# Optimization experiments

Hardware: AMD Instinct MI355X
Metric: run time of the kernel (lower is better)

Reference implementation:

```python
import jax, jax.numpy as jnp
import numpy as np
import math

B, N, D = 8, 2048, 64


def setup_inputs() -> dict:
    key = jax.random.key(0)
    kq, kk, kv, kd = jax.random.split(key, 4)
    Q = jax.random.normal(kq, (B, N, D), dtype=jnp.float32)
    K = jax.random.normal(kk, (B, N, D), dtype=jnp.float32)
    V = jax.random.normal(kv, (B, N, D), dtype=jnp.float32)
    dist_matrix = jax.random.uniform(kd, (N, N), dtype=jnp.float32)
    return {"Q": Q, "K": K, "V": V, "dist_matrix": dist_matrix}


def rescale_distance_matrix(dist_matrix):
    # (1 + e^1) / (1 + exp(1 - dist))
    c = 1.0
    return (c + math.e) / (c + jnp.exp(c - dist_matrix))


def reference(Q, K, V, dist_matrix):
    d_k = K.shape[-1]
    inv_sqrt_dk = 1.0 / math.sqrt(d_k)
    # [B, N, N] raw attention logits
    qk = jnp.einsum("bnd,bmd->bnm", Q, K)
    # ReLU then multiply by rescaled distance matrix [N, N] on the right
    scores = jnp.matmul(jax.nn.relu(qk), rescale_distance_matrix(dist_matrix)) * inv_sqrt_dk
    attn = jax.nn.softmax(scores, axis=-1)
    context = jnp.einsum("bnm,bmd->bnd", attn, V)
    return context
```

## Files before the change

kernel.cpp:

```cpp
#include <hip/hip_runtime.h>


typedef _Float16 f16;
typedef _Float16 f16x8 __attribute__((ext_vector_type(8)));
typedef float    f32x4 __attribute__((ext_vector_type(4)));

#define AS1C(p) ((const __attribute__((address_space(1))) void*)(p))
#define AS3(p)  ((__attribute__((address_space(3))) void*)(p))

__device__ __forceinline__ f16x8 cvt_f16x8(float4 a, float4 b){
  f16x8 v;
  v[0]=(f16)a.x; v[1]=(f16)a.y; v[2]=(f16)a.z; v[3]=(f16)a.w;
  v[4]=(f16)b.x; v[5]=(f16)b.y; v[6]=(f16)b.z; v[7]=(f16)b.w;
  return v;
}

__launch_bounds__(256, 2)
__global__ void k_qk(const float* __restrict__ Q, const float* __restrict__ Km,
                     const float* __restrict__ V, const float* __restrict__ Dm,
                     f16* __restrict__ Ph, f16* __restrict__ RhT,
                     f16* __restrict__ VhT){
  __shared__ char shm[36864];
  const int bid = blockIdx.x;
  const int t = threadIdx.x;

  if (bid >= 2048){
    f16* tl = (f16*)shm;
    const int c = t & 63, g = t >> 6;
    if (bid < 3072){
      const int pid = bid - 2048;
      const int k0 = (pid & 31)*64, m0 = (pid >> 5)*64;
#pragma unroll
      for (int i=0;i<16;++i){
        int k = g*16 + i;
        float d = Dm[(size_t)(k0 + k)*2048 + m0 + c];
        tl[k*65 + c] = (f16)(3.7182818284590452f / (1.0f + __expf(1.0f - d)));
      }
      __syncthreads();
#pragma unroll
      for (int i=0;i<16;++i){
        int m = g*16 + i;
        RhT[(size_t)(m0 + m)*2048 + k0 + c] = tl[c*65 + m];
      }
    } else {
      const int pid = bid - 3072;
      const int m0 = (pid & 31)*64, b = pid >> 5;
#pragma unroll
      for (int i=0;i<16;++i){
        int m = g*16 + i;
        tl[m*65 + c] = (f16)V[((size_t)b*2048 + m0 + m)*64 + c];
      }
      __syncthreads();
#pragma unroll
      for (int i=0;i<16;++i){
        int d = g*16 + i;
        VhT[((size_t)b*64 + d)*2048 + m0 + c] = tl[c*65 + d];
      }
    }
    return;
  }

  f16* Qt = (f16*)shm;
  f16* Kt = (f16*)(shm + 18432);
  f16* Tt = (f16*)shm;

  const int w = t>>6, l = t&63, lr = l&15, q = l>>4;
  const int m0 = (bid & 15)*128, n0 = ((bid>>4) & 15)*128, b = bid >> 8;
  const int wr = (w>>1)*64, wc = (w&1)*64;
  const float* Qb = Q  + ((size_t)b*2048 + n0)*64;
  const float* Kb = Km + ((size_t)b*2048 + m0)*64;

  const int sr = t>>3, sc = t&7;
#pragma unroll
  for (int j=0;j<4;++j){
    int row = sr + 32*j;
    const float* p  = Qb + (size_t)row*64 + sc*8;
    *(f16x8*)(Qt + row*72 + sc*8) = cvt_f16x8(*(const float4*)p, *(const float4*)(p+4));
    const float* pk = Kb + (size_t)row*64 + sc*8;
    *(f16x8*)(Kt + row*72 + sc*8) = cvt_f16x8(*(const float4*)pk, *(const float4*)(pk+4));
  }
  __syncthreads();

  f32x4 acc[4][4] = {};
#pragma unroll
  for (int kc=0;kc<2;++kc){
    f16x8 af[4], bf[4];
#pragma unroll
    for (int ti=0;ti<4;++ti) af[ti] = *(const f16x8*)(Qt + (wr+16*ti+lr)*72 + kc*32 + q*8);
#pragma unroll
    for (int tj=0;tj<4;++tj) bf[tj] = *(const f16x8*)(Kt + (wc+16*tj+lr)*72 + kc*32 + q*8);
#pragma unroll
    for (int ti=0;ti<4;++ti)
#pragma unroll
      for (int tj=0;tj<4;++tj)
        acc[ti][tj] = __builtin_amdgcn_mfma_f32_16x16x32_f16(af[ti], bf[tj], acc[ti][tj], 0,0,0);
  }
  __syncthreads();
#pragma unroll
  for (int ti=0;ti<4;++ti)
#pragma unroll
    for (int tj=0;tj<4;++tj)
#pragma unroll
      for (int r=0;r<4;++r)
        Tt[(wr+16*ti+4*q+r)*136 + wc+16*tj+lr] = (f16)(fmaxf(acc[ti][tj][r],0.f)*0.125f);
  __syncthreads();
  const int g16 = t&15, r0 = t>>4;
#pragma unroll
  for (int j=0;j<8;++j){
    int row = r0 + 16*j;
    *(f16x8*)(Ph + ((size_t)b*2048 + n0 + row)*2048 + m0 + g16*8) =
        *(const f16x8*)(Tt + row*136 + g16*8);
  }
}

__launch_bounds__(256, 2)
__global__ void k_attn(const f16* __restrict__ Ph, const f16* __restrict__ RhT,
                       const f16* __restrict__ VhT, f16* __restrict__ Op,
                       float* __restrict__ mp, float* __restrict__ lp){
  __shared__ char smem[49152];
  f16*  Pbuf = (f16*)smem;
  f16*  Rbuf = (f16*)(smem + 16384);
  f16*  El   = (f16*)smem;
  float* stat_max = (float*)(smem + 33792);
  float* stat_sum = (float*)(smem + 34816);

  const int t = threadIdx.x, w = t>>6, l = t&63, lr = l&15, q = l>>4;
  const int bid = blockIdx.x;
  const int jq = bid & 7, nbb = bid >> 3, b = nbb & 7, nb = nbb >> 3;
  const int n0 = nb*128, jg = jq*256;
  const int wc = w*64;

  const f16* Pblk = Ph  + ((size_t)b*2048 + n0)*2048;
  const f16* Vb   = VhT + (size_t)b*64*2048;

  const f16* srcP[2];
  const f16* srcR[4];
#pragma unroll
  for (int i=0;i<2;++i){
    int slot = i*256 + t, row = slot>>2, g = slot&3;
    srcP[i] = Pblk + (size_t)row*2048 + (g ^ ((row>>1)&3))*8;
  }
#pragma unroll
  for (int i=0;i<4;++i){
    int slot = i*256 + t, row = slot>>2, g = slot&3;
    srcR[i] = RhT + (size_t)(jg + row)*2048 + (g ^ ((row>>1)&3))*8;
  }

  auto stage = [&](int kc){
    const int cb = kc & 1, k0 = kc*32;
#pragma unroll
    for (int i=0;i<2;++i)
      __builtin_amdgcn_global_load_lds(AS1C(srcP[i] + k0),
                                       AS3(Pbuf + cb*4096 + i*2048 + w*512), 16, 0, 0);
#pragma unroll
    for (int i=0;i<4;++i)
      __builtin_amdgcn_global_load_lds(AS1C(srcR[i] + k0),
                                       AS3(Rbuf + cb*8192 + i*2048 + w*512), 16, 0, 0);
  };

  const int swz = (lr>>1)&3;
  f32x4 acc[8][4] = {};
  f32x4 Oacc[2][2][2] = {};

  stage(0);
#pragma unroll 2
  for (int kc = 0; kc < 64; ++kc){
    __syncthreads();
    if (kc < 63) stage(kc+1);
    const int cb = kc & 1;
    const f16* Pb = Pbuf + cb*4096;
    const f16* Rb = Rbuf + cb*8192;
    f16x8 bf[4];
#pragma unroll
    for (int tj=0;tj<4;++tj)
      bf[tj] = *(const f16x8*)(Rb + (wc + 16*tj + lr)*32 + (q ^ swz)*8);
#pragma unroll
    for (int ti=0;ti<8;++ti){
      f16x8 af = *(const f16x8*)(Pb + (16*ti + lr)*32 + (q ^ swz)*8);
#pragma unroll
      for (int tj=0;tj<4;++tj)
        acc[ti][tj] = __builtin_amdgcn_mfma_f32_16x16x32_f16(af, bf[tj], acc[ti][tj], 0,0,0);
    }
  }
  __syncthreads();

#pragma unroll
  for (int p=0;p<2;++p){
    float pm[4][4];
#pragma unroll
    for (int ti=0;ti<4;++ti)
#pragma unroll
      for (int r=0;r<4;++r)
        pm[ti][r] = fmaxf(fmaxf(acc[4*p+ti][0][r], acc[4*p+ti][1][r]),
                          fmaxf(acc[4*p+ti][2][r], acc[4*p+ti][3][r]));
#pragma unroll
    for (int mm=1;mm<16;mm<<=1)
#pragma unroll
      for (int ti=0;ti<4;++ti)
#pragma unroll
        for (int r=0;r<4;++r)
          pm[ti][r] = fmaxf(pm[ti][r], __shfl_xor(pm[ti][r], mm));
    if (lr == 0)
#pragma unroll
      for (int ti=0;ti<4;++ti)
#pragma unroll
        for (int r=0;r<4;++r)
          stat_max[(16*ti + 4*q + r)*4 + w] = pm[ti][r];
    __syncthreads();

    float Mn[4][4], ps[4][4];
#pragma unroll
    for (int ti=0;ti<4;++ti)
#pragma unroll
      for (int r=0;r<4;++r){
        int row = 16*ti + 4*q + r;
        float4 s4 = *(const float4*)&stat_max[row*4];
        Mn[ti][r] = fmaxf(fmaxf(s4.x,s4.y), fmaxf(s4.z,s4.w));
        ps[ti][r] = 0.f;
      }
#pragma unroll
    for (int ti=0;ti<4;++ti)
#pragma unroll
      for (int tj=0;tj<4;++tj)
#pragma unroll
        for (int r=0;r<4;++r){
          float e = __expf(acc[4*p+ti][tj][r] - Mn[ti][r]);
          ps[ti][r] += e;
          El[(16*ti + 4*q + r)*264 + wc + 16*tj + lr] = (f16)e;
        }
#pragma unroll
    for (int mm=1;mm<16;mm<<=1)
#pragma unroll
      for (int ti=0;ti<4;++ti)
#pragma unroll
        for (int r=0;r<4;++r)
          ps[ti][r] += __shfl_xor(ps[ti][r], mm);
    if (lr == 0)
#pragma unroll
      for (int ti=0;ti<4;++ti)
#pragma unroll
        for (int r=0;r<4;++r)
          stat_sum[(16*ti + 4*q + r)*4 + w] = ps[ti][r];
    __syncthreads();

    if (w == 0 && lr == 0)
#pragma unroll
      for (int ti=0;ti<4;++ti)
#pragma unroll
        for (int r=0;r<4;++r){
          int row = 16*ti + 4*q + r;
          float4 s4 = *(const float4*)&stat_sum[row*4];
          mp[bid*128 + 64*p + row] = Mn[ti][r];
          lp[bid*128 + 64*p + row] = s4.x + s4.y + s4.z + s4.w;
        }

    const int erb = 32*(w&1), vcb = 32*(w>>1);
#pragma unroll
    for (int ks=0; ks<8; ++ks){
      f16x8 ae[2], bv[2];
#pragma unroll
      for (int a=0;a<2;++a)
        ae[a] = *(const f16x8*)(El + (erb + 16*a + lr)*264 + ks*32 + q*8);
#pragma unroll
      for (int bb=0;bb<2;++bb)
        bv[bb] = *(const f16x8*)(Vb + (size_t)(vcb + 16*bb + lr)*2048 + jg + ks*32 + q*8);
#pragma unroll
      for (int a=0;a<2;++a)
#pragma unroll
        for (int bb=0;bb<2;++bb)
          Oacc[p][a][bb] = __builtin_amdgcn_mfma_f32_16x16x32_f16(ae[a], bv[bb], Oacc[p][a][bb], 0,0,0);
    }
    __syncthreads();
  }

#pragma unroll
  for (int p=0;p<2;++p)
#pragma unroll
    for (int a=0;a<2;++a)
#pragma unroll
      for (int bb=0;bb<2;++bb)
#pragma unroll
        for (int r=0;r<4;++r){
          int row = 64*p + 32*(w&1) + 16*a + 4*q + r;
          int col = 32*(w>>1) + 16*bb + lr;
          Op[((size_t)bid*128 + row)*64 + col] = (f16)Oacc[p][a][bb][r];
        }
}

__global__ void k_comb(const f16* __restrict__ Op, const float* __restrict__ mp,
                       const float* __restrict__ lp, float* __restrict__ out){
  const int rb = blockIdx.x;
  const int b = rb & 7, nb = rb >> 3;
  const int bid0 = rb << 3;
  const int t = threadIdx.x;
  const int row = t >> 1, half = t & 1;

  float m_[8], a_[8];
  float M = -1e30f, den = 0.f;
#pragma unroll
  for (int i=0;i<8;++i){ m_[i] = mp[(bid0+i)*128 + row]; M = fmaxf(M, m_[i]); }
#pragma unroll
  for (int i=0;i<8;++i){ a_[i] = __expf(m_[i] - M); den += a_[i]*lp[(bid0+i)*128 + row]; }
  float inv = 1.0f / den;

#pragma unroll
  for (int g=0;g<4;++g){
    int c0 = half*32 + g*8;
    float o[8] = {};
#pragma unroll
    for (int i=0;i<8;++i){
      f16x8 v = *(const f16x8*)(Op + ((size_t)(bid0+i)*128 + row)*64 + c0);
#pragma unroll
      for (int e=0;e<8;++e) o[e] += a_[i]*(float)v[e];
    }
    float4 o0, o1;
    o0.x=o[0]*inv; o0.y=o[1]*inv; o0.z=o[2]*inv; o0.w=o[3]*inv;
    o1.x=o[4]*inv; o1.y=o[5]*inv; o1.z=o[6]*inv; o1.w=o[7]*inv;
    float* dst = out + ((size_t)b*2048 + nb*128 + row)*64 + c0;
    *(float4*)dst = o0;
    *(float4*)(dst+4) = o1;
  }
}

extern "C" void kernel_launch(void* const* d_in, const int* in_sizes, int n_in,
                              void* d_out, int out_size, void* d_ws, size_t ws_size,
                              hipStream_t stream){
  (void)in_sizes; (void)n_in; (void)out_size; (void)ws_size;
  const float* Q  = (const float*)d_in[0];
  const float* K  = (const float*)d_in[1];
  const float* V  = (const float*)d_in[2];
  const float* Dm = (const float*)d_in[3];
  float* out = (float*)d_out;
  char* ws = (char*)d_ws;
  f16* Ph  = (f16*)ws;
  f16* RhT = (f16*)(ws + (size_t)64*1024*1024);
  f16* VhT = (f16*)(ws + (size_t)72*1024*1024);
  f16* Op  = (f16*)(ws + (size_t)74*1024*1024);
  float* mpp = (float*)(ws + (size_t)90*1024*1024);
  float* lpp = mpp + 1024*128;

  k_qk   <<<dim3(3328), 256, 0, stream>>>(Q, K, V, Dm, Ph, RhT, VhT);
  k_attn <<<dim3(1024), 256, 0, stream>>>(Ph, RhT, VhT, Op, mpp, lpp);
  k_comb <<<dim3(128),  256, 0, stream>>>(Op, mpp, lpp, out);
}
```

Baseline: 248.3 us.

## Use 32x32x16 MFMA for the P·R GEMM and widen the combine kernel grid

```diff
diff --git a/kernel.cpp b/kernel.cpp
--- a/kernel.cpp
+++ b/kernel.cpp
@@ -4,6 +4,7 @@
 typedef _Float16 f16;
 typedef _Float16 f16x8 __attribute__((ext_vector_type(8)));
 typedef float    f32x4 __attribute__((ext_vector_type(4)));
+typedef float    f32x16 __attribute__((ext_vector_type(16)));
 
 #define AS1C(p) ((const __attribute__((address_space(1))) void*)(p))
 #define AS3(p)  ((__attribute__((address_space(3))) void*)(p))
@@ -20,7 +21,7 @@
                      const float* __restrict__ V, const float* __restrict__ Dm,
                      f16* __restrict__ Ph, f16* __restrict__ RhT,
                      f16* __restrict__ VhT){
-  __shared__ char shm[36864];
+  __shared__ __align__(16) char shm[36864];
   const int bid = blockIdx.x;
   const int t = threadIdx.x;
 
@@ -117,7 +118,7 @@
 __global__ void k_attn(const f16* __restrict__ Ph, const f16* __restrict__ RhT,
                        const f16* __restrict__ VhT, f16* __restrict__ Op,
                        float* __restrict__ mp, float* __restrict__ lp){
-  __shared__ char smem[49152];
+  __shared__ __align__(16) char smem[49152];
   f16*  Pbuf = (f16*)smem;
   f16*  Rbuf = (f16*)(smem + 16384);
   f16*  El   = (f16*)smem;
@@ -125,6 +126,7 @@
   float* stat_sum = (float*)(smem + 34816);
 
   const int t = threadIdx.x, w = t>>6, l = t&63, lr = l&15, q = l>>4;
+  const int c31 = l&31, hi = l>>5;
   const int bid = blockIdx.x;
   const int jq = bid & 7, nbb = bid >> 3, b = nbb & 7, nb = nbb >> 3;
   const int n0 = nb*128, jg = jq*256;
@@ -158,8 +160,8 @@
                                        AS3(Rbuf + cb*8192 + i*2048 + w*512), 16, 0, 0);
   };
 
-  const int swz = (lr>>1)&3;
-  f32x4 acc[8][4] = {};
+  const int swz32 = (c31>>1)&3;
+  f32x16 acc32[4][2] = {};
   f32x4 Oacc[2][2][2] = {};
 
   stage(0);
@@ -170,87 +172,92 @@
     const int cb = kc & 1;
     const f16* Pb = Pbuf + cb*4096;
     const f16* Rb = Rbuf + cb*8192;
-    f16x8 bf[4];
-#pragma unroll
-    for (int tj=0;tj<4;++tj)
-      bf[tj] = *(const f16x8*)(Rb + (wc + 16*tj + lr)*32 + (q ^ swz)*8);
-#pragma unroll
-    for (int ti=0;ti<8;++ti){
-      f16x8 af = *(const f16x8*)(Pb + (16*ti + lr)*32 + (q ^ swz)*8);
-#pragma unroll
-      for (int tj=0;tj<4;++tj)
-        acc[ti][tj] = __builtin_amdgcn_mfma_f32_16x16x32_f16(af, bf[tj], acc[ti][tj], 0,0,0);
+    f16x8 bf[2][2];
+#pragma unroll
+    for (int ct=0;ct<2;++ct)
+#pragma unroll
+      for (int f=0;f<2;++f)
+        bf[ct][f] = *(const f16x8*)(Rb + (wc + 32*ct + c31)*32 + ((2*f+hi) ^ swz32)*8);
+#pragma unroll
+    for (int rt=0;rt<4;++rt){
+#pragma unroll
+      for (int f=0;f<2;++f){
+        f16x8 af = *(const f16x8*)(Pb + (32*rt + c31)*32 + ((2*f+hi) ^ swz32)*8);
+        acc32[rt][0] = __builtin_amdgcn_mfma_f32_32x32x16_f16(af, bf[0][f], acc32[rt][0], 0,0,0);
+        acc32[rt][1] = __builtin_amdgcn_mfma_f32_32x32x16_f16(af, bf[1][f], acc32[rt][1], 0,0,0);
+      }
     }
   }
   __syncthreads();
 
 #pragma unroll
   for (int p=0;p<2;++p){
-    float pm[4][4];
-#pragma unroll
-    for (int ti=0;ti<4;++ti)
-#pragma unroll
-      for (int r=0;r<4;++r)
-        pm[ti][r] = fmaxf(fmaxf(acc[4*p+ti][0][r], acc[4*p+ti][1][r]),
-                          fmaxf(acc[4*p+ti][2][r], acc[4*p+ti][3][r]));
-#pragma unroll
-    for (int mm=1;mm<16;mm<<=1)
-#pragma unroll
-      for (int ti=0;ti<4;++ti)
-#pragma unroll
-        for (int r=0;r<4;++r)
-          pm[ti][r] = fmaxf(pm[ti][r], __shfl_xor(pm[ti][r], mm));
-    if (lr == 0)
-#pragma unroll
-      for (int ti=0;ti<4;++ti)
-#pragma unroll
-        for (int r=0;r<4;++r)
-          stat_max[(16*ti + 4*q + r)*4 + w] = pm[ti][r];
+    float pm[2][16];
+#pragma unroll
+    for (int u=0;u<2;++u)
+#pragma unroll
+      for (int rg=0;rg<16;++rg)
+        pm[u][rg] = fmaxf(acc32[2*p+u][0][rg], acc32[2*p+u][1][rg]);
+#pragma unroll
+    for (int mm=1;mm<32;mm<<=1)
+#pragma unroll
+      for (int u=0;u<2;++u)
+#pragma unroll
+        for (int rg=0;rg<16;++rg)
+          pm[u][rg] = fmaxf(pm[u][rg], __shfl_xor(pm[u][rg], mm));
+    if (c31 == 0)
+#pragma unroll
+      for (int u=0;u<2;++u)
+#pragma unroll
+        for (int rg=0;rg<16;++rg){
+          int row = u*32 + (rg&3) + 8*(rg>>2) + 4*hi;
+          stat_max[row*4 + w] = pm[u][rg];
+        }
     __syncthreads();
 
-    float Mn[4][4], ps[4][4];
-#pragma unroll
-    for (int ti=0;ti<4;++ti)
-#pragma unroll
-      for (int r=0;r<4;++r){
-        int row = 16*ti + 4*q + r;
+    float Mn[2][16];
+#pragma unroll
+    for (int u=0;u<2;++u){
+      float ps[16];
+#pragma unroll
+      for (int rg=0;rg<16;++rg){
+        int row = u*32 + (rg&3) + 8*(rg>>2) + 4*hi;
         float4 s4 = *(const float4*)&stat_max[row*4];
-        Mn[ti][r] = fmaxf(fmaxf(s4.x,s4.y), fmaxf(s4.z,s4.w));
-        ps[ti][r] = 0.f;
-      }
-#pragma unroll
-    for (int ti=0;ti<4;++ti)
-#pragma unroll
-      for (int tj=0;tj<4;++tj)
-#pragma unroll
-        for (int r=0;r<4;++r){
-          float e = __expf(acc[4*p+ti][tj][r] - Mn[ti][r]);
-          ps[ti][r] += e;
-          El[(16*ti + 4*q + r)*264 + wc + 16*tj + lr] = (f16)e;
-        }
-#pragma unroll
-    for (int mm=1;mm<16;mm<<=1)
-#pragma unroll
-      for (int ti=0;ti<4;++ti)
-#pragma unroll
-        for (int r=0;r<4;++r)
-          ps[ti][r] += __shfl_xor(ps[ti][r], mm);
-    if (lr == 0)
-#pragma unroll
-      for (int ti=0;ti<4;++ti)
-#pragma unroll
-        for (int r=0;r<4;++r)
-          stat_sum[(16*ti + 4*q + r)*4 + w] = ps[ti][r];
+        Mn[u][rg] = fmaxf(fmaxf(s4.x,s4.y), fmaxf(s4.z,s4.w));
+        ps[rg] = 0.f;
+      }
+#pragma unroll
+      for (int rg=0;rg<16;++rg){
+        int row = u*32 + (rg&3) + 8*(rg>>2) + 4*hi;
+#pragma unroll
+        for (int ct=0;ct<2;++ct){
+          float e = __expf(acc32[2*p+u][ct][rg] - Mn[u][rg]);
+          ps[rg] += e;
+          El[row*264 + wc + ct*32 + c31] = (f16)e;
+        }
+      }
+#pragma unroll
+      for (int mm=1;mm<32;mm<<=1)
+#pragma unroll
+        for (int rg=0;rg<16;++rg)
+          ps[rg] += __shfl_xor(ps[rg], mm);
+      if (c31 == 0)
+#pragma unroll
+        for (int rg=0;rg<16;++rg){
+          int row = u*32 + (rg&3) + 8*(rg>>2) + 4*hi;
+          stat_sum[row*4 + w] = ps[rg];
+          if (w == 0) mp[bid*128 + 64*p + row] = Mn[u][rg];
+        }
+    }
     __syncthreads();
 
-    if (w == 0 && lr == 0)
-#pragma unroll
-      for (int ti=0;ti<4;++ti)
-#pragma unroll
-        for (int r=0;r<4;++r){
-          int row = 16*ti + 4*q + r;
+    if (w == 0 && c31 == 0)
+#pragma unroll
+      for (int u=0;u<2;++u)
+#pragma unroll
+        for (int rg=0;rg<16;++rg){
+          int row = u*32 + (rg&3) + 8*(rg>>2) + 4*hi;
           float4 s4 = *(const float4*)&stat_sum[row*4];
-          mp[bid*128 + 64*p + row] = Mn[ti][r];
           lp[bid*128 + 64*p + row] = s4.x + s4.y + s4.z + s4.w;
         }
 
@@ -289,11 +296,13 @@
 
 __global__ void k_comb(const f16* __restrict__ Op, const float* __restrict__ mp,
                        const float* __restrict__ lp, float* __restrict__ out){
-  const int rb = blockIdx.x;
+  const int rb = blockIdx.x >> 2;
+  const int qr = blockIdx.x & 3;
   const int b = rb & 7, nb = rb >> 3;
   const int bid0 = rb << 3;
   const int t = threadIdx.x;
-  const int row = t >> 1, half = t & 1;
+  const int row = qr*32 + (t >> 3);
+  const int c0 = (t & 7)*8;
 
   float m_[8], a_[8];
   float M = -1e30f, den = 0.f;
@@ -303,23 +312,19 @@
   for (int i=0;i<8;++i){ a_[i] = __expf(m_[i] - M); den += a_[i]*lp[(bid0+i)*128 + row]; }
   float inv = 1.0f / den;
 
-#pragma unroll
-  for (int g=0;g<4;++g){
-    int c0 = half*32 + g*8;
-    float o[8] = {};
-#pragma unroll
-    for (int i=0;i<8;++i){
-      f16x8 v = *(const f16x8*)(Op + ((size_t)(bid0+i)*128 + row)*64 + c0);
-#pragma unroll
-      for (int e=0;e<8;++e) o[e] += a_[i]*(float)v[e];
-    }
-    float4 o0, o1;
-    o0.x=o[0]*inv; o0.y=o[1]*inv; o0.z=o[2]*inv; o0.w=o[3]*inv;
-    o1.x=o[4]*inv; o1.y=o[5]*inv; o1.z=o[6]*inv; o1.w=o[7]*inv;
-    float* dst = out + ((size_t)b*2048 + nb*128 + row)*64 + c0;
-    *(float4*)dst = o0;
-    *(float4*)(dst+4) = o1;
-  }
+  float o[8] = {};
+#pragma unroll
+  for (int i=0;i<8;++i){
+    f16x8 v = *(const f16x8*)(Op + ((size_t)(bid0+i)*128 + row)*64 + c0);
+#pragma unroll
+    for (int e=0;e<8;++e) o[e] += a_[i]*(float)v[e];
+  }
+  float4 o0, o1;
+  o0.x=o[0]*inv; o0.y=o[1]*inv; o0.z=o[2]*inv; o0.w=o[3]*inv;
+  o1.x=o[4]*inv; o1.y=o[5]*inv; o1.z=o[6]*inv; o1.w=o[7]*inv;
+  float* dst = out + ((size_t)b*2048 + nb*128 + row)*64 + c0;
+  *(float4*)dst = o0;
+  *(float4*)(dst+4) = o1;
 }
 
 extern "C" void kernel_launch(void* const* d_in, const int* in_sizes, int n_in,
@@ -341,5 +346,5 @@
 
   k_qk   <<<dim3(3328), 256, 0, stream>>>(Q, K, V, Dm, Ph, RhT, VhT);
   k_attn <<<dim3(1024), 256, 0, stream>>>(Ph, RhT, VhT, Op, mpp, lpp);
-  k_comb <<<dim3(128),  256, 0, stream>>>(Op, mpp, lpp, out);
-}
+  k_comb <<<dim3(512),  256, 0, stream>>>(Op, mpp, lpp, out);
+}
```

After: 270.5 us. +9.0%, slower.
